# Kernel tuning notes

Measured on AMD Instinct MI355X. Metric: run time of the kernel, lower is better.

Reference implementation:

```python
import jax, jax.numpy as jnp
import numpy as np

N, E, D = 100000, 1600000, 128
BN_EPS = 1e-5


def setup_inputs() -> dict:
    key = jax.random.key(0)
    ks = jax.random.split(key, 8)
    x = jax.random.normal(ks[0], (N, D), dtype=jnp.float32)
    edge_index = jax.random.randint(ks[1], (2, E), 0, N, dtype=jnp.int64)
    edge_attr = jax.random.normal(ks[2], (E, D), dtype=jnp.float32)
    W1 = jax.random.normal(ks[3], (D, D), dtype=jnp.float32) / np.sqrt(D)
    b1 = jnp.zeros((D,), dtype=jnp.float32)
    gamma = jnp.ones((D,), dtype=jnp.float32)
    beta = jnp.zeros((D,), dtype=jnp.float32)
    W2 = jax.random.normal(ks[4], (D, D), dtype=jnp.float32) / np.sqrt(D)
    b2 = jnp.zeros((D,), dtype=jnp.float32)
    return {"x": x, "edge_index": edge_index, "edge_attr": edge_attr,
            "W1": W1, "b1": b1, "gamma": gamma, "beta": beta,
            "W2": W2, "b2": b2}


def reference(x, edge_index, edge_attr, W1, b1, gamma, beta, W2, b2):
    src = edge_index[0]  # j: message source
    dst = edge_index[1]  # i: aggregation target
    # per-edge message: ReLU(x_j + e_ij)  -> [E, D]
    msg = jax.nn.relu(x[src] + edge_attr)
    # scatter-sum to destination nodes -> [N, D]
    aggr = jax.ops.segment_sum(msg, dst, num_segments=x.shape[0])
    # GINEConv with eps=0: (1+eps)*x_i + aggr
    h = x + aggr
    # gin_nn: Linear -> ReLU -> BatchNorm1d (batch stats, training mode) -> Linear
    h = jax.nn.relu(h @ W1 + b1)
    mean = jnp.mean(h, axis=0)
    var = jnp.var(h, axis=0)
    h = (h - mean) * jax.lax.rsqrt(var + BN_EPS) * gamma + beta
    return h @ W2 + b2
```

## Files before the change

### kernel.cpp

```cpp
#include <hip/hip_runtime.h>

#define D 128
#define BN_EPS 1e-5f
#define SB 256
#define ST 256

typedef short s16x8 __attribute__((ext_vector_type(8)));
typedef short s16x4 __attribute__((ext_vector_type(4)));
typedef float f32x4 __attribute__((ext_vector_type(4)));
typedef int   i32x2 __attribute__((ext_vector_type(2)));

static __device__ __forceinline__ short f2bf(float f) {
    unsigned u = __builtin_bit_cast(unsigned, f);
    u += 0x7FFFu + ((u >> 16) & 1u);
    return (short)(u >> 16);
}
static __device__ __forceinline__ float bf2f(short s) {
    unsigned u = ((unsigned)(unsigned short)s) << 16;
    return __builtin_bit_cast(float, u);
}

static __device__ __forceinline__ int wslot(int k, int f) {
    int t = k >> 5, kg = (k >> 3) & 3, e = k & 7;
    int c = f >> 4, fl = f & 15;
    return (((t * 8 + c) * 64 + kg * 16 + fl) * 8) + e;
}

__global__ __launch_bounds__(256) void k_xcast(
    const float* __restrict__ x, short* __restrict__ xb, int total8)
{
    int i = blockIdx.x * 256 + threadIdx.x;
    if (i >= total8) return;
    const float* p = x + (size_t)i * 8;
    f32x4 lo = __builtin_nontemporal_load((const f32x4*)p);
    f32x4 hi = __builtin_nontemporal_load((const f32x4*)(p + 4));
    s16x8 o;
    o[0] = f2bf(lo[0]); o[1] = f2bf(lo[1]); o[2] = f2bf(lo[2]); o[3] = f2bf(lo[3]);
    o[4] = f2bf(hi[0]); o[5] = f2bf(hi[1]); o[6] = f2bf(hi[2]); o[7] = f2bf(hi[3]);
    *(s16x8*)(xb + (size_t)i * 8) = o;
}

__global__ __launch_bounds__(256) void k_hist(
    const int* __restrict__ ei, int* __restrict__ deg, int E)
{
    int e = blockIdx.x * 256 + threadIdx.x;
    if (e >= E) return;
    atomicAdd(&deg[ei[E + e]], 1);
}

__global__ __launch_bounds__(ST) void k_scanA(
    const int* __restrict__ deg, int* __restrict__ bsum, int N, int chunk)
{
    int b = blockIdx.x;
    int start = b * chunk, end = min(start + chunk, N);
    int s = 0;
    for (int i = start + threadIdx.x; i < end; i += ST) s += deg[i];
    __shared__ int red[ST];
    red[threadIdx.x] = s;
    __syncthreads();
    for (int o = ST / 2; o > 0; o >>= 1) {
        if (threadIdx.x < o) red[threadIdx.x] += red[threadIdx.x + o];
        __syncthreads();
    }
    if (threadIdx.x == 0) bsum[b] = red[0];
}

__global__ __launch_bounds__(SB) void k_scanB(int* __restrict__ bsum)
{
    __shared__ int tmp[SB];
    int t = threadIdx.x;
    int orig = bsum[t];
    tmp[t] = orig;
    __syncthreads();
    for (int o = 1; o < SB; o <<= 1) {
        int u = (t >= o) ? tmp[t - o] : 0;
        __syncthreads();
        tmp[t] += u;
        __syncthreads();
    }
    bsum[t] = tmp[t] - orig;
}

__global__ __launch_bounds__(ST) void k_scanC(
    const int* __restrict__ deg, const int* __restrict__ bsum,
    int* __restrict__ offs, int* __restrict__ cur, int N, int chunk)
{
    int b = blockIdx.x;
    int start = b * chunk, end = min(start + chunk, N);
    __shared__ int tmp[ST];
    __shared__ int carry;
    int t = threadIdx.x;
    if (t == 0) carry = bsum[b];
    __syncthreads();
    for (int i0 = start; i0 < end; i0 += ST) {
        int i = i0 + t;
        int v = (i < end) ? deg[i] : 0;
        tmp[t] = v;
        __syncthreads();
        for (int o = 1; o < ST; o <<= 1) {
            int u = (t >= o) ? tmp[t - o] : 0;
            __syncthreads();
            tmp[t] += u;
            __syncthreads();
        }
        int incl = tmp[t];
        int total = tmp[ST - 1];
        if (i < end) {
            int ex = carry + incl - v;
            offs[i] = ex;
            cur[i] = ex;
        }
        __syncthreads();
        if (t == 0) carry += total;
        __syncthreads();
    }
}

__global__ __launch_bounds__(256) void k_scatter(
    const int* __restrict__ ei, int* __restrict__ cur,
    int2* __restrict__ bucket, int E)
{
    int e = blockIdx.x * 256 + threadIdx.x;
    if (e >= E) return;
    int dst = ei[E + e];
    int pos = atomicAdd(&cur[dst], 1);
    bucket[pos] = make_int2(ei[e], e);
}

__global__ __launch_bounds__(256) void k_aggr(
    const short* __restrict__ xb, const float* __restrict__ ea,
    const int2* __restrict__ bucket, const int* __restrict__ offs,
    const int* __restrict__ deg, short* __restrict__ h, int N)
{
    int node = blockIdx.x * 16 + (threadIdx.x >> 4);
    if (node >= N) return;
    int lane = threadIdx.x & 15;
    int c0 = lane * 8;
    int start = offs[node];
    int d = deg[node];
    const int2* bp = bucket + start;

    float acc[8];
    {
        s16x8 xs = *(const s16x8*)(xb + (size_t)node * D + c0);
        #pragma unroll
        for (int i = 0; i < 8; ++i) acc[i] = bf2f(xs[i]);
    }

    int e = 0;
    for (; e + 4 <= d; e += 4) {
        i32x2 b[4];
        #pragma unroll
        for (int j = 0; j < 4; ++j)
            b[j] = __builtin_nontemporal_load((const i32x2*)(bp + e + j));
        s16x8 xv[4];
        f32x4 a0[4], a1[4];
        #pragma unroll
        for (int j = 0; j < 4; ++j) {
            xv[j] = *(const s16x8*)(xb + (size_t)b[j][0] * D + c0);
            const float* ap = ea + (size_t)b[j][1] * D + c0;
            a0[j] = __builtin_nontemporal_load((const f32x4*)ap);
            a1[j] = __builtin_nontemporal_load((const f32x4*)(ap + 4));
        }
        #pragma unroll
        for (int j = 0; j < 4; ++j) {
            #pragma unroll
            for (int i = 0; i < 4; ++i) {
                acc[i]     += fmaxf(bf2f(xv[j][i])     + a0[j][i], 0.f);
                acc[i + 4] += fmaxf(bf2f(xv[j][i + 4]) + a1[j][i], 0.f);
            }
        }
    }
    for (; e < d; ++e) {
        i32x2 b = __builtin_nontemporal_load((const i32x2*)(bp + e));
        s16x8 xv = *(const s16x8*)(xb + (size_t)b[0] * D + c0);
        const float* ap = ea + (size_t)b[1] * D + c0;
        f32x4 a0 = __builtin_nontemporal_load((const f32x4*)ap);
        f32x4 a1 = __builtin_nontemporal_load((const f32x4*)(ap + 4));
        #pragma unroll
        for (int i = 0; i < 4; ++i) {
            acc[i]     += fmaxf(bf2f(xv[i])     + a0[i], 0.f);
            acc[i + 4] += fmaxf(bf2f(xv[i + 4]) + a1[i], 0.f);
        }
    }
    s16x8 o;
    #pragma unroll
    for (int i = 0; i < 8; ++i) o[i] = f2bf(acc[i]);
    *(s16x8*)(h + (size_t)node * D + c0) = o;
}

__global__ __launch_bounds__(256) void k_packW(
    const float* __restrict__ W, short* __restrict__ wp)
{
    int gid = blockIdx.x * 256 + threadIdx.x;
    int f = gid & 127;
    int kb = gid >> 7;
    #pragma unroll
    for (int e = 0; e < 8; ++e) {
        int k = kb * 8 + e;
        wp[wslot(k, f)] = f2bf(W[k * D + f]);
    }
}

template<int RELU, int OBF>
__global__ __launch_bounds__(256) void k_mgemm(
    const short* __restrict__ hin, const short* __restrict__ wp,
    const float* __restrict__ bias, void* __restrict__ outp, int N)
{
    __shared__ __align__(16) short wB[D * D];
    int tid = threadIdx.x;
    #pragma unroll
    for (int i = 0; i < 8; ++i) {
        int q = i * 256 + tid;
        *(s16x8*)&wB[q * 8] = *(const s16x8*)&wp[q * 8];
    }
    __syncthreads();

    int wv = tid >> 6, l = tid & 63;
    int cl = l & 15, kg = l >> 4;
    int ntiles = (N + 15) >> 4;

    float4 bv[8];
    #pragma unroll
    for (int c = 0; c < 8; ++c) bv[c] = *(const float4*)&bias[c * 16 + kg * 4];

    for (int tile = blockIdx.x * 4 + wv; tile < ntiles; tile += gridDim.x * 4) {
        int row0 = tile * 16;
        int rowA = min(row0 + cl, N - 1);
        const short* ap = hin + (size_t)rowA * D + kg * 8;
        s16x8 rF[4];
        #pragma unroll
        for (int t = 0; t < 4; ++t)
            rF[t] = *(const s16x8*)(ap + t * 32);

        bool ok = (row0 + cl < N);
        size_t obase = (size_t)(row0 + cl) * D + kg * 4;
        #pragma unroll
        for (int c = 0; c < 8; ++c) {
            f32x4 acc = { bv[c].x, bv[c].y, bv[c].z, bv[c].w };
            #pragma unroll
            for (int t = 0; t < 4; ++t) {
                s16x8 wF = *(const s16x8*)&wB[((t * 8 + c) * 64 + l) * 8];
                acc = __builtin_amdgcn_mfma_f32_16x16x32_bf16(wF, rF[t], acc, 0, 0, 0);
            }
            if (RELU) {
                acc[0] = fmaxf(acc[0], 0.f); acc[1] = fmaxf(acc[1], 0.f);
                acc[2] = fmaxf(acc[2], 0.f); acc[3] = fmaxf(acc[3], 0.f);
            }
            if (ok) {
                if (OBF) {
                    s16x4 o = { f2bf(acc[0]), f2bf(acc[1]), f2bf(acc[2]), f2bf(acc[3]) };
                    *(s16x4*)((short*)outp + obase + c * 16) = o;
                } else {
                    *(float4*)((float*)outp + obase + c * 16) =
                        make_float4(acc[0], acc[1], acc[2], acc[3]);
                }
            }
        }
    }
}

__global__ __launch_bounds__(256) void k_stats(
    const short* __restrict__ h1, float* __restrict__ gsum,
    float* __restrict__ gsq, int N)
{
    __shared__ float ls[D], lq[D];
    int tid = threadIdx.x;
    if (tid < D) { ls[tid] = 0.f; lq[tid] = 0.f; }
    __syncthreads();
    int c0 = (tid & 15) * 8;
    float s[8], q[8];
    #pragma unroll
    for (int i = 0; i < 8; ++i) { s[i] = 0.f; q[i] = 0.f; }
    for (int r = blockIdx.x * 16 + (tid >> 4); r < N; r += gridDim.x * 16) {
        s16x8 v = *(const s16x8*)(h1 + (size_t)r * D + c0);
        #pragma unroll
        for (int i = 0; i < 8; ++i) {
            float f = bf2f(v[i]);
            s[i] += f; q[i] += f * f;
        }
    }
    #pragma unroll
    for (int i = 0; i < 8; ++i) {
        atomicAdd(&ls[c0 + i], s[i]);
        atomicAdd(&lq[c0 + i], q[i]);
    }
    __syncthreads();
    if (tid < D) {
        atomicAdd(&gsum[tid], ls[tid]);
        atomicAdd(&gsq[tid], lq[tid]);
    }
}

__global__ __launch_bounds__(128) void k_fold(
    const float* __restrict__ gsum, const float* __restrict__ gsq,
    const float* __restrict__ gamma, const float* __restrict__ beta,
    const float* __restrict__ W2, const float* __restrict__ b2,
    short* __restrict__ wp2, float* __restrict__ b2p, int N)
{
    __shared__ float sS[D], tS[D];
    int j = threadIdx.x;
    float invN = 1.0f / (float)N;
    float mean = gsum[j] * invN;
    float var = gsq[j] * invN - mean * mean;
    float rstd = rsqrtf(var + BN_EPS);
    float s = rstd * gamma[j];
    sS[j] = s;
    tS[j] = beta[j] - mean * s;
    __syncthreads();
    float acc = b2[j];
    #pragma unroll 4
    for (int k = 0; k < D; ++k) {
        float w = W2[k * D + j];
        wp2[wslot(k, j)] = f2bf(sS[k] * w);
        acc = fmaf(tS[k], w, acc);
    }
    b2p[j] = acc;
}

extern "C" void kernel_launch(void* const* d_in, const int* in_sizes, int n_in,
                              void* d_out, int out_size, void* d_ws, size_t ws_size,
                              hipStream_t stream) {
    const float* x     = (const float*)d_in[0];
    const int*   ei    = (const int*)d_in[1];
    const float* ea    = (const float*)d_in[2];
    const float* W1    = (const float*)d_in[3];
    const float* b1    = (const float*)d_in[4];
    const float* gamma = (const float*)d_in[5];
    const float* beta  = (const float*)d_in[6];
    const float* W2    = (const float*)d_in[7];
    const float* b2    = (const float*)d_in[8];
    float* out = (float*)d_out;

    int N = in_sizes[0] / D;
    int E = in_sizes[1] / 2;

    char* ws = (char*)d_ws;
    int2*  bucket = (int2*)ws;
    int*   deg    = (int*)(ws + (size_t)E * sizeof(int2));
    float* gsum   = (float*)(deg + N);
    float* gsq    = gsum + D;
    float* b2p    = gsq + D;
    int*   offs   = (int*)(b2p + D);
    int*   cur    = offs + N;
    int*   bsum   = cur + N;
    short* wp1    = (short*)(bsum + SB);
    short* wp2    = wp1 + D * D;
    short* xb     = wp2 + D * D;
    short* h      = xb + (size_t)N * D;
    short* h1     = h + (size_t)N * D;

    hipMemsetAsync(deg, 0, (size_t)N * sizeof(int) + 2 * D * sizeof(float), stream);

    int chunk = (N + SB - 1) / SB;
    int eB = (E + 255) / 256;
    int x8 = (N * D) / 8;

    k_xcast<<<(x8 + 255) / 256, 256, 0, stream>>>(x, xb, x8);
    k_hist<<<eB, 256, 0, stream>>>(ei, deg, E);
    k_scanA<<<SB, ST, 0, stream>>>(deg, bsum, N, chunk);
    k_scanB<<<1, SB, 0, stream>>>(bsum);
    k_scanC<<<SB, ST, 0, stream>>>(deg, bsum, offs, cur, N, chunk);
    k_scatter<<<eB, 256, 0, stream>>>(ei, cur, bucket, E);
    k_aggr<<<(N + 15) / 16, 256, 0, stream>>>(xb, ea, bucket, offs, deg, h, N);

    int ntiles = (N + 15) / 16;
    int gB = (ntiles + 7) / 8;
    k_packW<<<8, 256, 0, stream>>>(W1, wp1);
    k_mgemm<1, 1><<<gB, 256, 0, stream>>>(h, wp1, b1, h1, N);
    k_stats<<<512, 256, 0, stream>>>(h1, gsum, gsq, N);
    k_fold<<<1, 128, 0, stream>>>(gsum, gsq, gamma, beta, W2, b2, wp2, b2p, N);
    k_mgemm<0, 0><<<gB, 256, 0, stream>>>(h1, wp2, b2p, out, N);
}
```

Before: 521.6 us.

## Fuse BN stats into GEMM, merge scan stages, widen aggregation per node

Batch-norm column statistics are now accumulated inside the first GEMM epilogue from fp32 values and reduced with shuffles plus global atomics, which removes the separate stats pass over h1. The block-sum scan is folded into every scanC block, so one launch goes away at the cost of redundant work in each block. The aggregation kernel now gives each node a full wavefront, with four edge slots each handling 8 features and combined by a shuffle reduction, to expose more memory parallelism for low-degree nodes. Weight packing now writes vectorised stores, and k_fold's unroll factor is raised.

```diff
diff --git a/kernel.cpp b/kernel.cpp
--- a/kernel.cpp
+++ b/kernel.cpp
@@ -65,32 +65,25 @@
     if (threadIdx.x == 0) bsum[b] = red[0];
 }
 
-__global__ __launch_bounds__(SB) void k_scanB(int* __restrict__ bsum)
-{
-    __shared__ int tmp[SB];
-    int t = threadIdx.x;
-    int orig = bsum[t];
-    tmp[t] = orig;
-    __syncthreads();
-    for (int o = 1; o < SB; o <<= 1) {
-        int u = (t >= o) ? tmp[t - o] : 0;
-        __syncthreads();
-        tmp[t] += u;
-        __syncthreads();
-    }
-    bsum[t] = tmp[t] - orig;
-}
-
 __global__ __launch_bounds__(ST) void k_scanC(
     const int* __restrict__ deg, const int* __restrict__ bsum,
     int* __restrict__ offs, int* __restrict__ cur, int N, int chunk)
 {
     int b = blockIdx.x;
     int start = b * chunk, end = min(start + chunk, N);
+    __shared__ int btmp[SB];
     __shared__ int tmp[ST];
     __shared__ int carry;
     int t = threadIdx.x;
-    if (t == 0) carry = bsum[b];
+    btmp[t] = bsum[t];
+    __syncthreads();
+    for (int o = 1; o < SB; o <<= 1) {
+        int u = (t >= o) ? btmp[t - o] : 0;
+        __syncthreads();
+        btmp[t] += u;
+        __syncthreads();
+    }
+    if (t == 0) carry = (b == 0) ? 0 : btmp[b - 1];
     __syncthreads();
     for (int i0 = start; i0 < end; i0 += ST) {
         int i = i0 + t;
@@ -132,61 +125,60 @@
     const int2* __restrict__ bucket, const int* __restrict__ offs,
     const int* __restrict__ deg, short* __restrict__ h, int N)
 {
-    int node = blockIdx.x * 16 + (threadIdx.x >> 4);
+    int node = blockIdx.x * 4 + (threadIdx.x >> 6);
     if (node >= N) return;
-    int lane = threadIdx.x & 15;
-    int c0 = lane * 8;
+    int lane = threadIdx.x & 63;
+    int es = lane >> 4;
+    int fl = lane & 15;
+    int c0 = fl * 8;
     int start = offs[node];
     int d = deg[node];
     const int2* bp = bucket + start;
 
-    float acc[8];
-    {
+    f32x4 acc0 = {0.f, 0.f, 0.f, 0.f};
+    f32x4 acc1 = {0.f, 0.f, 0.f, 0.f};
+
+    for (int e = 0; e < d; e += 8) {
+        int e0 = e + es, e1 = e + 4 + es;
+        bool v0 = e0 < d, v1 = e1 < d;
+        int i0 = min(e0, d - 1), i1 = min(e1, d - 1);
+        i32x2 b0 = __builtin_nontemporal_load((const i32x2*)(bp + i0));
+        i32x2 b1 = __builtin_nontemporal_load((const i32x2*)(bp + i1));
+        s16x8 x0 = *(const s16x8*)(xb + (size_t)b0[0] * D + c0);
+        s16x8 x1 = *(const s16x8*)(xb + (size_t)b1[0] * D + c0);
+        const float* ap0 = ea + (size_t)b0[1] * D + c0;
+        const float* ap1 = ea + (size_t)b1[1] * D + c0;
+        f32x4 a00 = __builtin_nontemporal_load((const f32x4*)ap0);
+        f32x4 a01 = __builtin_nontemporal_load((const f32x4*)(ap0 + 4));
+        f32x4 a10 = __builtin_nontemporal_load((const f32x4*)ap1);
+        f32x4 a11 = __builtin_nontemporal_load((const f32x4*)(ap1 + 4));
+        #pragma unroll
+        for (int i = 0; i < 4; ++i) {
+            float m00 = fmaxf(bf2f(x0[i])     + a00[i], 0.f);
+            float m01 = fmaxf(bf2f(x0[i + 4]) + a01[i], 0.f);
+            float m10 = fmaxf(bf2f(x1[i])     + a10[i], 0.f);
+            float m11 = fmaxf(bf2f(x1[i + 4]) + a11[i], 0.f);
+            acc0[i] += (v0 ? m00 : 0.f) + (v1 ? m10 : 0.f);
+            acc1[i] += (v0 ? m01 : 0.f) + (v1 ? m11 : 0.f);
+        }
+    }
+    #pragma unroll
+    for (int i = 0; i < 4; ++i) {
+        acc0[i] += __shfl_xor(acc0[i], 16);
+        acc0[i] += __shfl_xor(acc0[i], 32);
+        acc1[i] += __shfl_xor(acc1[i], 16);
+        acc1[i] += __shfl_xor(acc1[i], 32);
+    }
+    if (es == 0) {
         s16x8 xs = *(const s16x8*)(xb + (size_t)node * D + c0);
-        #pragma unroll
-        for (int i = 0; i < 8; ++i) acc[i] = bf2f(xs[i]);
-    }
-
-    int e = 0;
-    for (; e + 4 <= d; e += 4) {
-        i32x2 b[4];
-        #pragma unroll
-        for (int j = 0; j < 4; ++j)
-            b[j] = __builtin_nontemporal_load((const i32x2*)(bp + e + j));
-        s16x8 xv[4];
-        f32x4 a0[4], a1[4];
-        #pragma unroll
-        for (int j = 0; j < 4; ++j) {
-            xv[j] = *(const s16x8*)(xb + (size_t)b[j][0] * D + c0);
-            const float* ap = ea + (size_t)b[j][1] * D + c0;
-            a0[j] = __builtin_nontemporal_load((const f32x4*)ap);
-            a1[j] = __builtin_nontemporal_load((const f32x4*)(ap + 4));
-        }
-        #pragma unroll
-        for (int j = 0; j < 4; ++j) {
-            #pragma unroll
-            for (int i = 0; i < 4; ++i) {
-                acc[i]     += fmaxf(bf2f(xv[j][i])     + a0[j][i], 0.f);
-                acc[i + 4] += fmaxf(bf2f(xv[j][i + 4]) + a1[j][i], 0.f);
-            }
-        }
-    }
-    for (; e < d; ++e) {
-        i32x2 b = __builtin_nontemporal_load((const i32x2*)(bp + e));
-        s16x8 xv = *(const s16x8*)(xb + (size_t)b[0] * D + c0);
-        const float* ap = ea + (size_t)b[1] * D + c0;
-        f32x4 a0 = __builtin_nontemporal_load((const f32x4*)ap);
-        f32x4 a1 = __builtin_nontemporal_load((const f32x4*)(ap + 4));
+        s16x8 o;
         #pragma unroll
         for (int i = 0; i < 4; ++i) {
-            acc[i]     += fmaxf(bf2f(xv[i])     + a0[i], 0.f);
-            acc[i + 4] += fmaxf(bf2f(xv[i + 4]) + a1[i], 0.f);
-        }
-    }
-    s16x8 o;
-    #pragma unroll
-    for (int i = 0; i < 8; ++i) o[i] = f2bf(acc[i]);
-    *(s16x8*)(h + (size_t)node * D + c0) = o;
+            o[i]     = f2bf(acc0[i] + bf2f(xs[i]));
+            o[i + 4] = f2bf(acc1[i] + bf2f(xs[i + 4]));
+        }
+        *(s16x8*)(h + (size_t)node * D + c0) = o;
+    }
 }
 
 __global__ __launch_bounds__(256) void k_packW(
@@ -195,17 +187,18 @@
     int gid = blockIdx.x * 256 + threadIdx.x;
     int f = gid & 127;
     int kb = gid >> 7;
+    s16x8 o;
     #pragma unroll
-    for (int e = 0; e < 8; ++e) {
-        int k = kb * 8 + e;
-        wp[wslot(k, f)] = f2bf(W[k * D + f]);
-    }
+    for (int e = 0; e < 8; ++e)
+        o[e] = f2bf(W[(kb * 8 + e) * D + f]);
+    *(s16x8*)&wp[wslot(kb * 8, f)] = o;
 }
 
 template<int RELU, int OBF>
 __global__ __launch_bounds__(256) void k_mgemm(
     const short* __restrict__ hin, const short* __restrict__ wp,
-    const float* __restrict__ bias, void* __restrict__ outp, int N)
+    const float* __restrict__ bias, void* __restrict__ outp,
+    float* __restrict__ gsum, float* __restrict__ gsq, int N)
 {
     __shared__ __align__(16) short wB[D * D];
     int tid = threadIdx.x;
@@ -223,6 +216,12 @@
     float4 bv[8];
     #pragma unroll
     for (int c = 0; c < 8; ++c) bv[c] = *(const float4*)&bias[c * 16 + kg * 4];
+
+    f32x4 sc[8], sq[8];
+    if (RELU) {
+        #pragma unroll
+        for (int c = 0; c < 8; ++c) { sc[c] = {0.f,0.f,0.f,0.f}; sq[c] = {0.f,0.f,0.f,0.f}; }
+    }
 
     for (int tile = blockIdx.x * 4 + wv; tile < ntiles; tile += gridDim.x * 4) {
         int row0 = tile * 16;
@@ -246,6 +245,13 @@
             if (RELU) {
                 acc[0] = fmaxf(acc[0], 0.f); acc[1] = fmaxf(acc[1], 0.f);
                 acc[2] = fmaxf(acc[2], 0.f); acc[3] = fmaxf(acc[3], 0.f);
+                if (ok) {
+                    #pragma unroll
+                    for (int r = 0; r < 4; ++r) {
+                        sc[c][r] += acc[r];
+                        sq[c][r] += acc[r] * acc[r];
+                    }
+                }
             }
             if (ok) {
                 if (OBF) {
@@ -258,37 +264,23 @@
             }
         }
     }
-}
-
-__global__ __launch_bounds__(256) void k_stats(
-    const short* __restrict__ h1, float* __restrict__ gsum,
-    float* __restrict__ gsq, int N)
-{
-    __shared__ float ls[D], lq[D];
-    int tid = threadIdx.x;
-    if (tid < D) { ls[tid] = 0.f; lq[tid] = 0.f; }
-    __syncthreads();
-    int c0 = (tid & 15) * 8;
-    float s[8], q[8];
-    #pragma unroll
-    for (int i = 0; i < 8; ++i) { s[i] = 0.f; q[i] = 0.f; }
-    for (int r = blockIdx.x * 16 + (tid >> 4); r < N; r += gridDim.x * 16) {
-        s16x8 v = *(const s16x8*)(h1 + (size_t)r * D + c0);
-        #pragma unroll
-        for (int i = 0; i < 8; ++i) {
-            float f = bf2f(v[i]);
-            s[i] += f; q[i] += f * f;
-        }
-    }
-    #pragma unroll
-    for (int i = 0; i < 8; ++i) {
-        atomicAdd(&ls[c0 + i], s[i]);
-        atomicAdd(&lq[c0 + i], q[i]);
-    }
-    __syncthreads();
-    if (tid < D) {
-        atomicAdd(&gsum[tid], ls[tid]);
-        atomicAdd(&gsq[tid], lq[tid]);
+
+    if (RELU) {
+        #pragma unroll
+        for (int c = 0; c < 8; ++c) {
+            #pragma unroll
+            for (int r = 0; r < 4; ++r) {
+                float s = sc[c][r], q = sq[c][r];
+                s += __shfl_xor(s, 1); s += __shfl_xor(s, 2);
+                s += __shfl_xor(s, 4); s += __shfl_xor(s, 8);
+                q += __shfl_xor(q, 1); q += __shfl_xor(q, 2);
+                q += __shfl_xor(q, 4); q += __shfl_xor(q, 8);
+                if (cl == 0) {
+                    atomicAdd(&gsum[c * 16 + kg * 4 + r], s);
+                    atomicAdd(&gsq[c * 16 + kg * 4 + r], q);
+                }
+            }
+        }
     }
 }
 
@@ -309,7 +301,7 @@
     tS[j] = beta[j] - mean * s;
     __syncthreads();
     float acc = b2[j];
-    #pragma unroll 4
+    #pragma unroll 8
     for (int k = 0; k < D; ++k) {
         float w = W2[k * D + j];
         wp2[wslot(k, j)] = f2bf(sS[k] * w);
@@ -359,16 +351,14 @@
     k_xcast<<<(x8 + 255) / 256, 256, 0, stream>>>(x, xb, x8);
     k_hist<<<eB, 256, 0, stream>>>(ei, deg, E);
     k_scanA<<<SB, ST, 0, stream>>>(deg, bsum, N, chunk);
-    k_scanB<<<1, SB, 0, stream>>>(bsum);
     k_scanC<<<SB, ST, 0, stream>>>(deg, bsum, offs, cur, N, chunk);
     k_scatter<<<eB, 256, 0, stream>>>(ei, cur, bucket, E);
-    k_aggr<<<(N + 15) / 16, 256, 0, stream>>>(xb, ea, bucket, offs, deg, h, N);
+    k_aggr<<<(N + 3) / 4, 256, 0, stream>>>(xb, ea, bucket, offs, deg, h, N);
 
     int ntiles = (N + 15) / 16;
     int gB = (ntiles + 7) / 8;
     k_packW<<<8, 256, 0, stream>>>(W1, wp1);
-    k_mgemm<1, 1><<<gB, 256, 0, stream>>>(h, wp1, b1, h1, N);
-    k_stats<<<512, 256, 0, stream>>>(h1, gsum, gsq, N);
+    k_mgemm<1, 1><<<gB, 256, 0, stream>>>(h, wp1, b1, h1, gsum, gsq, N);
     k_fold<<<1, 128, 0, stream>>>(gsum, gsq, gamma, beta, W2, b2, wp2, b2p, N);
-    k_mgemm<0, 0><<<gB, 256, 0, stream>>>(h1, wp2, b2p, out, N);
-}
+    k_mgemm<0, 0><<<gB, 256, 0, stream>>>(h1, wp2, b2p, out, gsum, gsq, N);
+}
```

New measurement: 787.7 us. 51.0% more time.
